# Kernel tuning notes

Measured on AMD Instinct MI355X. Metric: run time of the kernel, lower is better.

The kernel has to match this reference:

```python
import jax, jax.numpy as jnp
import numpy as np

H = 30  # hidden size
D_IN = 4
D_OUT = 4


def setup_inputs() -> dict:
    key = jax.random.key(0)
    ks = jax.random.split(key, 12)
    s = 0.1
    inp = {
        "input": jax.random.normal(ks[0], (2048, 1024, D_IN), dtype=jnp.float32),
        "W_ih1": jax.random.normal(ks[1], (4 * H, D_IN), dtype=jnp.float32) * s,
        "b_ih1": jax.random.normal(ks[2], (4 * H,), dtype=jnp.float32) * s,
        "W_hh1": jax.random.normal(ks[3], (4 * H, H), dtype=jnp.float32) * s,
        "b_hh1": jax.random.normal(ks[4], (4 * H,), dtype=jnp.float32) * s,
        "W_ih2": jax.random.normal(ks[5], (4 * H, H), dtype=jnp.float32) * s,
        "b_ih2": jax.random.normal(ks[6], (4 * H,), dtype=jnp.float32) * s,
        "W_hh2": jax.random.normal(ks[7], (4 * H, H), dtype=jnp.float32) * s,
        "b_hh2": jax.random.normal(ks[8], (4 * H,), dtype=jnp.float32) * s,
        "W_lin": jax.random.normal(ks[9], (D_OUT, H), dtype=jnp.float32) * s,
        "b_lin": jax.random.normal(ks[10], (D_OUT,), dtype=jnp.float32) * s,
        "future": 0,
    }
    return inp


def _lstm_cell(x, h, c, W_ih, b_ih, W_hh, b_hh):
    # PyTorch LSTMCell gate order: i, f, g, o
    gates = x @ W_ih.T + b_ih + h @ W_hh.T + b_hh  # [B, 4H]
    i, f, g, o = jnp.split(gates, 4, axis=-1)
    i = jax.nn.sigmoid(i)
    f = jax.nn.sigmoid(f)
    g = jnp.tanh(g)
    o = jax.nn.sigmoid(o)
    c_new = f * c + i * g
    h_new = o * jnp.tanh(c_new)
    return h_new, c_new


def reference(input, W_ih1, b_ih1, W_hh1, b_hh1, W_ih2, b_ih2, W_hh2, b_hh2,
              W_lin, b_lin, future):
    B, T, _ = input.shape

    def step(carry, x_t):
        h1, c1, h2, c2 = carry
        h1, c1 = _lstm_cell(x_t[:, :D_IN], h1, c1, W_ih1, b_ih1, W_hh1, b_hh1)
        h2, c2 = _lstm_cell(h1, h2, c2, W_ih2, b_ih2, W_hh2, b_hh2)
        out = h2 @ W_lin.T + b_lin  # [B, 4]
        return (h1, c1, h2, c2), out

    z = jnp.zeros((B, H), dtype=input.dtype)
    carry0 = (z, z, z, z)
    carry, outs = jax.lax.scan(step, carry0, jnp.transpose(input, (1, 0, 2)))
    outputs = jnp.transpose(outs, (1, 0, 2))  # [B, T, 4]

    if future > 0:
        h1, c1, h2, c2 = carry
        out = outputs[:, -1, :]
        fut = []
        for _ in range(future):
            h1, c1 = _lstm_cell(out, h1, c1, W_ih1, b_ih1, W_hh1, b_hh1)
            h2, c2 = _lstm_cell(h1, h2, c2, W_ih2, b_ih2, W_hh2, b_hh2)
            out = h2 @ W_lin.T + b_lin
            fut.append(out)
        outputs = jnp.concatenate([outputs, jnp.stack(fut, axis=1)], axis=1)
    return outputs
```

## Files before the change

kernel.cpp:

```cpp
#include <hip/hip_runtime.h>

typedef float f32x4 __attribute__((ext_vector_type(4)));
typedef float v4f  __attribute__((ext_vector_type(4)));
typedef _Float16 half8 __attribute__((ext_vector_type(8)));
typedef unsigned int u32;
typedef unsigned short u16;

#define HH 30
#define DIN 4
#define DOUT 4
#define NB 16
#define L2E 1.44269504088896340736f

#if __has_builtin(__builtin_amdgcn_exp2f)
#define EXP2F(v) __builtin_amdgcn_exp2f(v)
#else
#define EXP2F(v) exp2f(v)
#endif

__device__ __forceinline__ float sig2f(float v) {
    return __builtin_amdgcn_rcpf(1.0f + EXP2F(v));
}

__device__ __forceinline__ f32x4 MF(half8 a, half8 b, f32x4 c) {
    return __builtin_amdgcn_mfma_f32_16x16x32_f16(a, b, c, 0, 0, 0);
}

union F8 { half8 h; _Float16 e[8]; u32 w[4]; };
union HU { _Float16 h; u16 s; };

__device__ __forceinline__ void lds_barrier() {
    __builtin_amdgcn_sched_barrier(0);
    asm volatile("s_waitcnt lgkmcnt(0)" ::: "memory");
    __builtin_amdgcn_sched_barrier(0);
    __builtin_amdgcn_s_barrier();
    __builtin_amdgcn_sched_barrier(0);
}

__global__ __launch_bounds__(512)
void lstm2_kernel(const float* __restrict__ x,
                  const float* __restrict__ Wih1, const float* __restrict__ bih1,
                  const float* __restrict__ Whh1, const float* __restrict__ bhh1,
                  const float* __restrict__ Wih2, const float* __restrict__ bih2,
                  const float* __restrict__ Whh2, const float* __restrict__ bhh2,
                  const float* __restrict__ Wlin, const float* __restrict__ blin,
                  float* __restrict__ out, int T)
{
    const int tid = threadIdx.x;
    const int w = tid >> 6;
    const int l = tid & 63;
    const int n = l & 15;
    const int p = l >> 4;
    const int b0 = blockIdx.x * NB;
    const float M2 = -2.0f * L2E;

    __shared__ __align__(16) u16 lds[2][4][16][40];

    {
        u32* z = reinterpret_cast<u32*>(&lds[0][0][0][0]);
        const int tot = 2 * 4 * 16 * 40 / 2;
        for (int i = tid; i < tot; i += 512) z[i] = 0u;
    }

    const int gA = n & 3;
    const float scA = (gA == 2) ? -2.0f * L2E : -L2E;
    const int qA = 4 * w + (n >> 2);

    half8 a1h_h, a1h_l;
    half8 a1x_h, a1x_l;
    half8 a2i_h, a2i_l;
    half8 a2h_h, a2h_l;
    {
        F8 Hh, Hl, Xh, Xl, Ih, Il, Rh, Rl;
#pragma unroll
        for (int e = 0; e < 8; ++e) {
            const int k = 16 * (e >> 2) + 4 * p + (e & 3);
            float v; _Float16 t16;
            v = (qA < HH && k < HH) ? Whh1[(gA * HH + qA) * HH + k] * scA : 0.0f;
            t16 = (_Float16)v; Hh.e[e] = t16; Hl.e[e] = (_Float16)(v - (float)t16);
            v = (qA < HH && k < DIN) ? Wih1[(gA * HH + qA) * DIN + k] * scA : 0.0f;
            t16 = (_Float16)v; Xh.e[e] = t16; Xl.e[e] = (_Float16)(v - (float)t16);
            v = (qA < HH && k < HH) ? Wih2[(gA * HH + qA) * HH + k] * scA : 0.0f;
            t16 = (_Float16)v; Ih.e[e] = t16; Il.e[e] = (_Float16)(v - (float)t16);
            v = (qA < HH && k < HH) ? Whh2[(gA * HH + qA) * HH + k] * scA : 0.0f;
            t16 = (_Float16)v; Rh.e[e] = t16; Rl.e[e] = (_Float16)(v - (float)t16);
        }
        a1h_h = Hh.h; a1h_l = Hl.h;
        a1x_h = Xh.h; a1x_l = Xl.h;
        a2i_h = Ih.h; a2i_l = Il.h;
        a2h_h = Rh.h; a2h_l = Rl.h;
    }

    const int kq = 4 * w + p;
    const bool okq = (kq < HH);
    const int pos = ((kq & 15) >> 2) * 8 + (kq >> 4) * 4 + (kq & 3);

    f32x4 bias1f, bias2f;
#pragma unroll
    for (int r = 0; r < 4; ++r) {
        const float scr = (r == 2) ? -2.0f * L2E : -L2E;
        bias1f[r] = okq ? (bih1[r * HH + kq] + bhh1[r * HH + kq]) * scr : 0.0f;
        bias2f[r] = okq ? (bih2[r * HH + kq] + bhh2[r * HH + kq]) * scr : 0.0f;
    }

    half8 alin_h, alin_l;
    f32x4 blinf;
    {
        F8 Lh, Ll;
#pragma unroll
        for (int e = 0; e < 8; ++e) {
            const int k = 16 * (e >> 2) + 4 * p + (e & 3);
            float v = (n < DOUT && k < HH) ? Wlin[n * HH + k] : 0.0f;
            _Float16 t16 = (_Float16)v;
            Lh.e[e] = t16; Ll.e[e] = (_Float16)(v - (float)t16);
        }
        alin_h = Lh.h; alin_l = Ll.h;
#pragma unroll
        for (int r = 0; r < 4; ++r)
            blinf[r] = (p == 0) ? blin[r] : 0.0f;
    }

    float c1 = 0.0f, c2 = 0.0f;
    half8 bh1_h, bh1_l, bh2_h, bh2_l;

    const v4f* xp = reinterpret_cast<const v4f*>(x) + (size_t)(b0 + n) * T;
    const v4f x0 = xp[0];

    __syncthreads();

    {
        F8 XH, XL;
#pragma unroll
        for (int e = 0; e < 8; ++e) { XH.e[e] = (_Float16)0.0f; XL.e[e] = (_Float16)0.0f; }
        if (p == 0) {
#pragma unroll
            for (int e = 0; e < 4; ++e) {
                _Float16 t16 = (_Float16)x0[e];
                XH.e[e] = t16; XL.e[e] = (_Float16)(x0[e] - (float)t16);
            }
        }
        f32x4 g1 = bias1f;
        g1 = MF(a1x_h, XH.h, g1);
        g1 = MF(a1x_h, XL.h, g1);
        g1 = MF(a1x_l, XH.h, g1);
        const float iv = sig2f(g1[0]);
        const float fv = sig2f(g1[1]);
        const float gg = fmaf(2.0f, sig2f(g1[2]), -1.0f);
        const float ov = sig2f(g1[3]);
        c1 = fmaf(fv, c1, iv * gg);
        const float h1n = ov * fmaf(2.0f, sig2f(M2 * c1), -1.0f);
        HU hi, lo;
        hi.h = (_Float16)h1n;
        lo.h = (_Float16)(h1n - (float)hi.h);
        lds[0][0][n][pos] = okq ? hi.s : (u16)0;
        lds[0][1][n][pos] = okq ? lo.s : (u16)0;
    }
    __syncthreads();
    bh1_h = *reinterpret_cast<const half8*>(&lds[0][0][n][8 * p]);
    bh1_l = *reinterpret_cast<const half8*>(&lds[0][1][n][8 * p]);
    bh2_h = *reinterpret_cast<const half8*>(&lds[0][2][n][8 * p]);
    bh2_l = *reinterpret_cast<const half8*>(&lds[0][3][n][8 * p]);

    half8 bx_h, bx_l;
    {
        const v4f x1 = xp[(T > 1) ? 1 : 0];
        F8 XH, XL;
#pragma unroll
        for (int e = 0; e < 8; ++e) { XH.e[e] = (_Float16)0.0f; XL.e[e] = (_Float16)0.0f; }
        if (p == 0) {
#pragma unroll
            for (int e = 0; e < 4; ++e) {
                _Float16 t16 = (_Float16)x1[e];
                XH.e[e] = t16; XL.e[e] = (_Float16)(x1[e] - (float)t16);
            }
        }
        bx_h = XH.h; bx_l = XL.h;
    }
    v4f xn = xp[(T > 2) ? 2 : (T - 1)];

    const f32x4 zf = {0.0f, 0.0f, 0.0f, 0.0f};

    for (int t = 0; t < T; ++t) {
        f32x4 g2a = bias2f;
        g2a = MF(a2i_h, bh1_h, g2a);
        g2a = MF(a2i_h, bh1_l, g2a);
        g2a = MF(a2i_l, bh1_h, g2a);
        f32x4 g2b = zf;
        g2b = MF(a2h_h, bh2_h, g2b);
        g2b = MF(a2h_h, bh2_l, g2b);
        g2b = MF(a2h_l, bh2_h, g2b);
        const f32x4 g2 = g2a + g2b;
        f32x4 g1a = bias1f;
        g1a = MF(a1h_h, bh1_h, g1a);
        g1a = MF(a1h_h, bh1_l, g1a);
        g1a = MF(a1h_l, bh1_h, g1a);
        f32x4 g1b = zf;
        g1b = MF(a1x_h, bx_h, g1b);
        g1b = MF(a1x_h, bx_l, g1b);
        g1b = MF(a1x_l, bx_h, g1b);
        const f32x4 g1 = g1a + g1b;

        const float iv2 = sig2f(g2[0]);
        const float fv2 = sig2f(g2[1]);
        const float gg2 = fmaf(2.0f, sig2f(g2[2]), -1.0f);
        const float ov2 = sig2f(g2[3]);
        c2 = fmaf(fv2, c2, iv2 * gg2);
        const float h2n = ov2 * fmaf(2.0f, sig2f(M2 * c2), -1.0f);

        const float iv1 = sig2f(g1[0]);
        const float fv1 = sig2f(g1[1]);
        const float gg1 = fmaf(2.0f, sig2f(g1[2]), -1.0f);
        const float ov1 = sig2f(g1[3]);
        c1 = fmaf(fv1, c1, iv1 * gg1);
        const float h1n = ov1 * fmaf(2.0f, sig2f(M2 * c1), -1.0f);

        const int bw = (t + 1) & 1;
        HU h1hi, h1lo, h2hi, h2lo;
        h1hi.h = (_Float16)h1n;
        h1lo.h = (_Float16)(h1n - (float)h1hi.h);
        h2hi.h = (_Float16)h2n;
        h2lo.h = (_Float16)(h2n - (float)h2hi.h);
        lds[bw][0][n][pos] = okq ? h1hi.s : (u16)0;
        lds[bw][1][n][pos] = okq ? h1lo.s : (u16)0;
        lds[bw][2][n][pos] = okq ? h2hi.s : (u16)0;
        lds[bw][3][n][pos] = okq ? h2lo.s : (u16)0;

        lds_barrier();

        bh1_h = *reinterpret_cast<const half8*>(&lds[bw][0][n][8 * p]);
        bh1_l = *reinterpret_cast<const half8*>(&lds[bw][1][n][8 * p]);
        bh2_h = *reinterpret_cast<const half8*>(&lds[bw][2][n][8 * p]);
        bh2_l = *reinterpret_cast<const half8*>(&lds[bw][3][n][8 * p]);

        {
            F8 XH, XL;
#pragma unroll
            for (int e = 0; e < 8; ++e) { XH.e[e] = (_Float16)0.0f; XL.e[e] = (_Float16)0.0f; }
            if (p == 0) {
#pragma unroll
                for (int e = 0; e < 4; ++e) {
                    _Float16 t16 = (_Float16)xn[e];
                    XH.e[e] = t16; XL.e[e] = (_Float16)(xn[e] - (float)t16);
                }
            }
            bx_h = XH.h; bx_l = XL.h;
        }
        xn = xp[(t + 3 < T) ? (t + 3) : (T - 1)];

        if (w == 7) {
            f32x4 oh = blinf;
            oh = MF(alin_h, bh2_h, oh);
            oh = MF(alin_h, bh2_l, oh);
            oh = MF(alin_l, bh2_h, oh);
            if (p == 0) {
                v4f ov;
                ov.x = oh[0]; ov.y = oh[1]; ov.z = oh[2]; ov.w = oh[3];
                *reinterpret_cast<v4f*>(out + (((size_t)(b0 + n)) * T + t) * DOUT) = ov;
            }
        }
    }
}

extern "C" void kernel_launch(void* const* d_in, const int* in_sizes, int n_in,
                              void* d_out, int out_size, void* d_ws, size_t ws_size,
                              hipStream_t stream)
{
    const float* x    = (const float*)d_in[0];
    const float* Wih1 = (const float*)d_in[1];
    const float* bih1 = (const float*)d_in[2];
    const float* Whh1 = (const float*)d_in[3];
    const float* bhh1 = (const float*)d_in[4];
    const float* Wih2 = (const float*)d_in[5];
    const float* bih2 = (const float*)d_in[6];
    const float* Whh2 = (const float*)d_in[7];
    const float* bhh2 = (const float*)d_in[8];
    const float* Wlin = (const float*)d_in[9];
    const float* blin = (const float*)d_in[10];
    float* out = (float*)d_out;

    const int T = 1024;
    const int B = in_sizes[0] / (T * DIN);

    hipLaunchKernelGGL(lstm2_kernel, dim3(B / NB), dim3(512), 0, stream,
                       x, Wih1, bih1, Whh1, bhh1, Wih2, bih2, Whh2, bhh2,
                       Wlin, blin, out, T);
}
```

Measured before the change: 762.0 us.

## Split LSTM layers across separate wave groups with a skewed layer pipeline

Doubles the block to 1024 threads. Waves 0-7 run layer 1 and waves 8-15 run layer 2 one step behind, so each wave carries fewer MFMA chains per step. The input projection for layer 1 moves from fp16-split MFMAs to scalar FMAs computed ahead of time, and the output projection rotates across the layer-2 waves. The cost is two extra pipeline steps, a 1024-thread barrier every step, and lower occupancy per CU, since 128 blocks of 16 waves fit on fewer CUs.

```diff
diff --git a/kernel.cpp b/kernel.cpp
--- a/kernel.cpp
+++ b/kernel.cpp
@@ -37,7 +37,7 @@
     __builtin_amdgcn_sched_barrier(0);
 }
 
-__global__ __launch_bounds__(512)
+__global__ __launch_bounds__(1024)
 void lstm2_kernel(const float* __restrict__ x,
                   const float* __restrict__ Wih1, const float* __restrict__ bih1,
                   const float* __restrict__ Whh1, const float* __restrict__ bhh1,
@@ -48,6 +48,8 @@
 {
     const int tid = threadIdx.x;
     const int w = tid >> 6;
+    const int wt = w & 7;
+    const bool isL2 = (w >= 8);
     const int l = tid & 63;
     const int n = l & 15;
     const int p = l >> 4;
@@ -55,52 +57,58 @@
     const float M2 = -2.0f * L2E;
 
     __shared__ __align__(16) u16 lds[2][4][16][40];
-
     {
         u32* z = reinterpret_cast<u32*>(&lds[0][0][0][0]);
         const int tot = 2 * 4 * 16 * 40 / 2;
-        for (int i = tid; i < tot; i += 512) z[i] = 0u;
+        for (int i = tid; i < tot; i += 1024) z[i] = 0u;
     }
 
     const int gA = n & 3;
     const float scA = (gA == 2) ? -2.0f * L2E : -L2E;
-    const int qA = 4 * w + (n >> 2);
-
-    half8 a1h_h, a1h_l;
-    half8 a1x_h, a1x_l;
-    half8 a2i_h, a2i_l;
-    half8 a2h_h, a2h_l;
+    const int qA = 4 * wt + (n >> 2);
+    const int kq = 4 * wt + p;
+    const bool okq = (kq < HH);
+    const int kqc = okq ? kq : 0;
+    const int pos = ((kq & 15) >> 2) * 8 + (kq >> 4) * 4 + (kq & 3);
+
+    half8 wA_h0, wA_l0, wA_h1, wA_l1;
     {
-        F8 Hh, Hl, Xh, Xl, Ih, Il, Rh, Rl;
+        F8 H0, L0, H1, L1v;
 #pragma unroll
         for (int e = 0; e < 8; ++e) {
             const int k = 16 * (e >> 2) + 4 * p + (e & 3);
-            float v; _Float16 t16;
-            v = (qA < HH && k < HH) ? Whh1[(gA * HH + qA) * HH + k] * scA : 0.0f;
-            t16 = (_Float16)v; Hh.e[e] = t16; Hl.e[e] = (_Float16)(v - (float)t16);
-            v = (qA < HH && k < DIN) ? Wih1[(gA * HH + qA) * DIN + k] * scA : 0.0f;
-            t16 = (_Float16)v; Xh.e[e] = t16; Xl.e[e] = (_Float16)(v - (float)t16);
-            v = (qA < HH && k < HH) ? Wih2[(gA * HH + qA) * HH + k] * scA : 0.0f;
-            t16 = (_Float16)v; Ih.e[e] = t16; Il.e[e] = (_Float16)(v - (float)t16);
-            v = (qA < HH && k < HH) ? Whh2[(gA * HH + qA) * HH + k] * scA : 0.0f;
-            t16 = (_Float16)v; Rh.e[e] = t16; Rl.e[e] = (_Float16)(v - (float)t16);
-        }
-        a1h_h = Hh.h; a1h_l = Hl.h;
-        a1x_h = Xh.h; a1x_l = Xl.h;
-        a2i_h = Ih.h; a2i_l = Il.h;
-        a2h_h = Rh.h; a2h_l = Rl.h;
-    }
-
-    const int kq = 4 * w + p;
-    const bool okq = (kq < HH);
-    const int pos = ((kq & 15) >> 2) * 8 + (kq >> 4) * 4 + (kq & 3);
-
-    f32x4 bias1f, bias2f;
+            const bool kok = (qA < HH && k < HH);
+            float v0, v1;
+            if (isL2) {
+                v0 = kok ? Wih2[(gA * HH + qA) * HH + k] * scA : 0.0f;
+                v1 = kok ? Whh2[(gA * HH + qA) * HH + k] * scA : 0.0f;
+            } else {
+                v0 = kok ? Whh1[(gA * HH + qA) * HH + k] * scA : 0.0f;
+                v1 = 0.0f;
+            }
+            _Float16 t0 = (_Float16)v0, t1 = (_Float16)v1;
+            H0.e[e] = t0; L0.e[e] = (_Float16)(v0 - (float)t0);
+            H1.e[e] = t1; L1v.e[e] = (_Float16)(v1 - (float)t1);
+        }
+        wA_h0 = H0.h; wA_l0 = L0.h; wA_h1 = H1.h; wA_l1 = L1v.h;
+    }
+
+    f32x4 biasf;
 #pragma unroll
     for (int r = 0; r < 4; ++r) {
         const float scr = (r == 2) ? -2.0f * L2E : -L2E;
-        bias1f[r] = okq ? (bih1[r * HH + kq] + bhh1[r * HH + kq]) * scr : 0.0f;
-        bias2f[r] = okq ? (bih2[r * HH + kq] + bhh2[r * HH + kq]) * scr : 0.0f;
+        const float bv = isL2 ? (bih2[r * HH + kqc] + bhh2[r * HH + kqc])
+                              : (bih1[r * HH + kqc] + bhh1[r * HH + kqc]);
+        biasf[r] = okq ? bv * scr : 0.0f;
+    }
+
+    float wxs[4][DIN];
+#pragma unroll
+    for (int r = 0; r < 4; ++r) {
+        const float scr = (r == 2) ? -2.0f * L2E : -L2E;
+#pragma unroll
+        for (int c = 0; c < DIN; ++c)
+            wxs[r][c] = (!isL2 && okq) ? Wih1[(r * HH + kqc) * DIN + c] * scr : 0.0f;
     }
 
     half8 alin_h, alin_l;
@@ -110,7 +118,7 @@
 #pragma unroll
         for (int e = 0; e < 8; ++e) {
             const int k = 16 * (e >> 2) + 4 * p + (e & 3);
-            float v = (n < DOUT && k < HH) ? Wlin[n * HH + k] : 0.0f;
+            float v = (isL2 && n < DOUT && k < HH) ? Wlin[n * HH + k] : 0.0f;
             _Float16 t16 = (_Float16)v;
             Lh.e[e] = t16; Ll.e[e] = (_Float16)(v - (float)t16);
         }
@@ -120,143 +128,102 @@
             blinf[r] = (p == 0) ? blin[r] : 0.0f;
     }
 
-    float c1 = 0.0f, c2 = 0.0f;
-    half8 bh1_h, bh1_l, bh2_h, bh2_l;
+    float cst = 0.0f;
+    half8 bh1_h = {}, bh1_l = {}, bh2_h = {}, bh2_l = {};
 
     const v4f* xp = reinterpret_cast<const v4f*>(x) + (size_t)(b0 + n) * T;
-    const v4f x0 = xp[0];
+
+    f32x4 gx_cur = biasf;
+    v4f xn = {};
+    if (!isL2) {
+        const v4f x0 = xp[0];
+#pragma unroll
+        for (int r = 0; r < 4; ++r)
+#pragma unroll
+            for (int c = 0; c < DIN; ++c)
+                gx_cur[r] = fmaf(wxs[r][c], x0[c], gx_cur[r]);
+        xn = xp[(T > 1) ? 1 : 0];
+    }
 
     __syncthreads();
 
-    {
-        F8 XH, XL;
-#pragma unroll
-        for (int e = 0; e < 8; ++e) { XH.e[e] = (_Float16)0.0f; XL.e[e] = (_Float16)0.0f; }
-        if (p == 0) {
-#pragma unroll
-            for (int e = 0; e < 4; ++e) {
-                _Float16 t16 = (_Float16)x0[e];
-                XH.e[e] = t16; XL.e[e] = (_Float16)(x0[e] - (float)t16);
+    const f32x4 zf = {0.0f, 0.0f, 0.0f, 0.0f};
+    const int TS = T + 2;
+
+    for (int s = 0; s < TS; ++s) {
+        if (!isL2) {
+            f32x4 a = MF(wA_h0, bh1_h, gx_cur);
+            f32x4 b = MF(wA_h0, bh1_l, zf);
+            f32x4 c = MF(wA_l0, bh1_h, zf);
+            const f32x4 g = (a + b) + c;
+
+            const float iv = sig2f(g[0]);
+            const float fv = sig2f(g[1]);
+            const float gg = fmaf(2.0f, sig2f(g[2]), -1.0f);
+            const float ov = sig2f(g[3]);
+            cst = fmaf(fv, cst, iv * gg);
+            const float r = sig2f(M2 * cst);
+            const float hn = fmaf(2.0f * ov, r, -ov);
+
+            HU hi, lo;
+            hi.h = (_Float16)hn;
+            lo.h = (_Float16)(hn - (float)hi.h);
+            lds[s & 1][0][n][pos] = okq ? hi.s : (u16)0;
+            lds[s & 1][1][n][pos] = okq ? lo.s : (u16)0;
+        } else {
+            if (s >= 1) {
+                f32x4 a = MF(wA_h0, bh1_h, biasf);
+                f32x4 b = MF(wA_h0, bh1_l, zf);
+                f32x4 c = MF(wA_l0, bh1_h, zf);
+                f32x4 d = MF(wA_h1, bh2_h, zf);
+                f32x4 e = MF(wA_h1, bh2_l, zf);
+                f32x4 f = MF(wA_l1, bh2_h, zf);
+                const f32x4 g = ((a + b) + (c + d)) + (e + f);
+
+                const float iv = sig2f(g[0]);
+                const float fv = sig2f(g[1]);
+                const float gg = fmaf(2.0f, sig2f(g[2]), -1.0f);
+                const float ov = sig2f(g[3]);
+                cst = fmaf(fv, cst, iv * gg);
+                const float r = sig2f(M2 * cst);
+                const float hn = fmaf(2.0f * ov, r, -ov);
+
+                HU hi, lo;
+                hi.h = (_Float16)hn;
+                lo.h = (_Float16)(hn - (float)hi.h);
+                lds[(s + 1) & 1][2][n][pos] = okq ? hi.s : (u16)0;
+                lds[(s + 1) & 1][3][n][pos] = okq ? lo.s : (u16)0;
             }
-        }
-        f32x4 g1 = bias1f;
-        g1 = MF(a1x_h, XH.h, g1);
-        g1 = MF(a1x_h, XL.h, g1);
-        g1 = MF(a1x_l, XH.h, g1);
-        const float iv = sig2f(g1[0]);
-        const float fv = sig2f(g1[1]);
-        const float gg = fmaf(2.0f, sig2f(g1[2]), -1.0f);
-        const float ov = sig2f(g1[3]);
-        c1 = fmaf(fv, c1, iv * gg);
-        const float h1n = ov * fmaf(2.0f, sig2f(M2 * c1), -1.0f);
-        HU hi, lo;
-        hi.h = (_Float16)h1n;
-        lo.h = (_Float16)(h1n - (float)hi.h);
-        lds[0][0][n][pos] = okq ? hi.s : (u16)0;
-        lds[0][1][n][pos] = okq ? lo.s : (u16)0;
-    }
-    __syncthreads();
-    bh1_h = *reinterpret_cast<const half8*>(&lds[0][0][n][8 * p]);
-    bh1_l = *reinterpret_cast<const half8*>(&lds[0][1][n][8 * p]);
-    bh2_h = *reinterpret_cast<const half8*>(&lds[0][2][n][8 * p]);
-    bh2_l = *reinterpret_cast<const half8*>(&lds[0][3][n][8 * p]);
-
-    half8 bx_h, bx_l;
-    {
-        const v4f x1 = xp[(T > 1) ? 1 : 0];
-        F8 XH, XL;
-#pragma unroll
-        for (int e = 0; e < 8; ++e) { XH.e[e] = (_Float16)0.0f; XL.e[e] = (_Float16)0.0f; }
-        if (p == 0) {
-#pragma unroll
-            for (int e = 0; e < 4; ++e) {
-                _Float16 t16 = (_Float16)x1[e];
-                XH.e[e] = t16; XL.e[e] = (_Float16)(x1[e] - (float)t16);
-            }
-        }
-        bx_h = XH.h; bx_l = XL.h;
-    }
-    v4f xn = xp[(T > 2) ? 2 : (T - 1)];
-
-    const f32x4 zf = {0.0f, 0.0f, 0.0f, 0.0f};
-
-    for (int t = 0; t < T; ++t) {
-        f32x4 g2a = bias2f;
-        g2a = MF(a2i_h, bh1_h, g2a);
-        g2a = MF(a2i_h, bh1_l, g2a);
-        g2a = MF(a2i_l, bh1_h, g2a);
-        f32x4 g2b = zf;
-        g2b = MF(a2h_h, bh2_h, g2b);
-        g2b = MF(a2h_h, bh2_l, g2b);
-        g2b = MF(a2h_l, bh2_h, g2b);
-        const f32x4 g2 = g2a + g2b;
-        f32x4 g1a = bias1f;
-        g1a = MF(a1h_h, bh1_h, g1a);
-        g1a = MF(a1h_h, bh1_l, g1a);
-        g1a = MF(a1h_l, bh1_h, g1a);
-        f32x4 g1b = zf;
-        g1b = MF(a1x_h, bx_h, g1b);
-        g1b = MF(a1x_h, bx_l, g1b);
-        g1b = MF(a1x_l, bx_h, g1b);
-        const f32x4 g1 = g1a + g1b;
-
-        const float iv2 = sig2f(g2[0]);
-        const float fv2 = sig2f(g2[1]);
-        const float gg2 = fmaf(2.0f, sig2f(g2[2]), -1.0f);
-        const float ov2 = sig2f(g2[3]);
-        c2 = fmaf(fv2, c2, iv2 * gg2);
-        const float h2n = ov2 * fmaf(2.0f, sig2f(M2 * c2), -1.0f);
-
-        const float iv1 = sig2f(g1[0]);
-        const float fv1 = sig2f(g1[1]);
-        const float gg1 = fmaf(2.0f, sig2f(g1[2]), -1.0f);
-        const float ov1 = sig2f(g1[3]);
-        c1 = fmaf(fv1, c1, iv1 * gg1);
-        const float h1n = ov1 * fmaf(2.0f, sig2f(M2 * c1), -1.0f);
-
-        const int bw = (t + 1) & 1;
-        HU h1hi, h1lo, h2hi, h2lo;
-        h1hi.h = (_Float16)h1n;
-        h1lo.h = (_Float16)(h1n - (float)h1hi.h);
-        h2hi.h = (_Float16)h2n;
-        h2lo.h = (_Float16)(h2n - (float)h2hi.h);
-        lds[bw][0][n][pos] = okq ? h1hi.s : (u16)0;
-        lds[bw][1][n][pos] = okq ? h1lo.s : (u16)0;
-        lds[bw][2][n][pos] = okq ? h2hi.s : (u16)0;
-        lds[bw][3][n][pos] = okq ? h2lo.s : (u16)0;
-
-        lds_barrier();
-
-        bh1_h = *reinterpret_cast<const half8*>(&lds[bw][0][n][8 * p]);
-        bh1_l = *reinterpret_cast<const half8*>(&lds[bw][1][n][8 * p]);
-        bh2_h = *reinterpret_cast<const half8*>(&lds[bw][2][n][8 * p]);
-        bh2_l = *reinterpret_cast<const half8*>(&lds[bw][3][n][8 * p]);
-
-        {
-            F8 XH, XL;
-#pragma unroll
-            for (int e = 0; e < 8; ++e) { XH.e[e] = (_Float16)0.0f; XL.e[e] = (_Float16)0.0f; }
-            if (p == 0) {
-#pragma unroll
-                for (int e = 0; e < 4; ++e) {
-                    _Float16 t16 = (_Float16)xn[e];
-                    XH.e[e] = t16; XL.e[e] = (_Float16)(xn[e] - (float)t16);
+            if (s >= 2 && w == 8 + (s & 7)) {
+                f32x4 oh = blinf;
+                oh = MF(alin_h, bh2_h, oh);
+                oh = MF(alin_h, bh2_l, oh);
+                oh = MF(alin_l, bh2_h, oh);
+                if (p == 0) {
+                    v4f ov4;
+                    ov4.x = oh[0]; ov4.y = oh[1]; ov4.z = oh[2]; ov4.w = oh[3];
+                    *reinterpret_cast<v4f*>(
+                        out + (((size_t)(b0 + n)) * T + (s - 2)) * DOUT) = ov4;
                 }
             }
-            bx_h = XH.h; bx_l = XL.h;
-        }
-        xn = xp[(t + 3 < T) ? (t + 3) : (T - 1)];
-
-        if (w == 7) {
-            f32x4 oh = blinf;
-            oh = MF(alin_h, bh2_h, oh);
-            oh = MF(alin_h, bh2_l, oh);
-            oh = MF(alin_l, bh2_h, oh);
-            if (p == 0) {
-                v4f ov;
-                ov.x = oh[0]; ov.y = oh[1]; ov.z = oh[2]; ov.w = oh[3];
-                *reinterpret_cast<v4f*>(out + (((size_t)(b0 + n)) * T + t) * DOUT) = ov;
-            }
+        }
+
+        lds_barrier();
+
+        bh1_h = *reinterpret_cast<const half8*>(&lds[s & 1][0][n][8 * p]);
+        bh1_l = *reinterpret_cast<const half8*>(&lds[s & 1][1][n][8 * p]);
+        if (isL2) {
+            bh2_h = *reinterpret_cast<const half8*>(&lds[(s + 1) & 1][2][n][8 * p]);
+            bh2_l = *reinterpret_cast<const half8*>(&lds[(s + 1) & 1][3][n][8 * p]);
+        } else {
+            f32x4 gxn = biasf;
+#pragma unroll
+            for (int r = 0; r < 4; ++r)
+#pragma unroll
+                for (int c = 0; c < DIN; ++c)
+                    gxn[r] = fmaf(wxs[r][c], xn[c], gxn[r]);
+            gx_cur = gxn;
+            xn = xp[(s + 2 < T) ? (s + 2) : (T - 1)];
         }
     }
 }
@@ -281,7 +248,7 @@
     const int T = 1024;
     const int B = in_sizes[0] / (T * DIN);
 
-    hipLaunchKernelGGL(lstm2_kernel, dim3(B / NB), dim3(512), 0, stream,
+    hipLaunchKernelGGL(lstm2_kernel, dim3(B / NB), dim3(1024), 0, stream,
                        x, Wih1, bih1, Whh1, bhh1, Wih2, bih2, Whh2, bhh2,
                        Wlin, blin, out, T);
 }
```

Measured after the change: 743.4 us. 1.03x faster.
